# Kernel optimization log

Measured on AMD Instinct MI355X. Metric: run time of the kernel, lower is better.

Reference implementation:

```python
import jax, jax.numpy as jnp
import numpy as np

WS = 8        # window_size
SHIFT = 4     # shift_size
DS = 16       # d_state
DTR = 4       # dt_rank = ceil(hidden_dim/16)


def _win_part(x, ws):
    # (B,H,W,C) -> (B*nH*nW, ws*ws, C)
    B, H, W, C = x.shape
    x = x.reshape(B, H // ws, ws, W // ws, ws, C).transpose(0, 1, 3, 2, 4, 5)
    return x.reshape(-1, ws * ws, C)


def _win_rev(xw, ws, B, H, W):
    C = xw.shape[-1]
    x = xw.reshape(B, H // ws, W // ws, ws, ws, C).transpose(0, 1, 3, 2, 4, 5)
    return x.reshape(B, H, W, C)


def _ln(x, g, b):
    mu = x.mean(-1, keepdims=True)
    var = x.var(-1, keepdims=True)
    return (x - mu) / jnp.sqrt(var + 1e-5) * g + b


def _conv2d(v, w, b, pad):
    out = jax.lax.conv_general_dilated(v, w, (1, 1), [(pad, pad), (pad, pad)],
                                       dimension_numbers=('NCHW', 'OIHW', 'NCHW'))
    return out + b[None, :, None, None]


def setup_inputs() -> dict:
    key = jax.random.key(0)
    B, C, H, W = 2, 64, 192, 192
    di = 128  # expand * hidden_dim
    ks = jax.random.split(key, 12)

    def n(k, shape, s=0.02):
        return jax.random.normal(k, shape, jnp.float32) * s

    return {
        'x': jax.random.normal(ks[0], (B, C, H, W), jnp.float32),
        'ln1_g': jnp.ones((C,), jnp.float32), 'ln1_b': jnp.zeros((C,), jnp.float32),
        'in_w': n(ks[1], (C, 2 * di)), 'in_b': jnp.zeros((2 * di,), jnp.float32),
        'conv_w': n(ks[2], (4, di), 0.1), 'conv_b': jnp.zeros((di,), jnp.float32),
        'xproj_w': n(ks[3], (di, DTR + 2 * DS)),
        'dt_w': n(ks[4], (DTR, di), 0.1),
        'dt_b': jnp.full((di,), float(np.log(np.expm1(0.01))), jnp.float32),
        'A_log': jnp.log(jnp.tile(jnp.arange(1, DS + 1, dtype=jnp.float32), (di, 1))),
        'D': jnp.ones((di,), jnp.float32),
        'out_w': n(ks[5], (di, C)), 'out_b': jnp.zeros((C,), jnp.float32),
        'skip1': jnp.ones((C,), jnp.float32),
        'ln2_g': jnp.ones((C,), jnp.float32), 'ln2_b': jnp.zeros((C,), jnp.float32),
        'skip2': jnp.ones((C,), jnp.float32),
        'cab_w1': n(ks[6], (C // 4, C, 3, 3), 0.05), 'cab_b1': jnp.zeros((C // 4,), jnp.float32),
        'cab_w2': n(ks[7], (C, C // 4, 3, 3), 0.05), 'cab_b2': jnp.zeros((C,), jnp.float32),
        'ca_wd': n(ks[8], (C // 16, C, 1, 1), 0.05), 'ca_bd': jnp.zeros((C // 16,), jnp.float32),
        'ca_wu': n(ks[9], (C, C // 16, 1, 1), 0.05), 'ca_bu': jnp.zeros((C,), jnp.float32),
    }


def reference(x, ln1_g, ln1_b, in_w, in_b, conv_w, conv_b, xproj_w, dt_w, dt_b,
              A_log, D, out_w, out_b, skip1, ln2_g, ln2_b, skip2,
              cab_w1, cab_b1, cab_w2, cab_b2, ca_wd, ca_bd, ca_wu, ca_bu):
    B, C, H, W = x.shape
    shortcut = x.transpose(0, 2, 3, 1)  # (B,H,W,C)
    # H,W divisible by WS -> no padding, pad mask is None
    xp = jnp.roll(shortcut, (-SHIFT, -SHIFT), axis=(1, 2))
    shift_mask = jnp.zeros((B, H, W, 1), x.dtype).at[:, :H - SHIFT, :W - SHIFT, :].set(1.0)
    mask_w = _win_part(shift_mask, WS)  # (N, L, 1)

    xn = _ln(xp, ln1_g, ln1_b)
    # --- SW_HSS3D: windowed Mamba selective-scan mixer ---
    xz = xn @ in_w + in_b
    x_in, z = jnp.split(xz, 2, axis=-1)
    xw = _win_part(x_in, WS) * mask_w        # (N, L, di)
    zw = _win_part(z, WS)
    K = conv_w.shape[0]
    L = xw.shape[1]
    xpad = jnp.pad(xw, ((0, 0), (K - 1, 0), (0, 0)))  # causal depthwise conv1d
    xc = sum(xpad[:, k:k + L, :] * conv_w[k] for k in range(K)) + conv_b
    xc = jax.nn.silu(xc)
    dbc = xc @ xproj_w
    dt = jax.nn.softplus(dbc[..., :DTR] @ dt_w + dt_b)  # (N,L,di)
    Bm = dbc[..., DTR:DTR + DS]
    Cm = dbc[..., DTR + DS:]
    A = -jnp.exp(A_log)  # (di,DS)

    def step(h, t):
        dt_t, B_t, C_t, x_t = t
        h = jnp.exp(dt_t[..., None] * A) * h + (dt_t * x_t)[..., None] * B_t[:, None, :]
        y = jnp.einsum('nds,ns->nd', h, C_t)
        return h, y

    N, di = xc.shape[0], xc.shape[-1]
    h0 = jnp.zeros((N, di, DS), xc.dtype)
    xs = (dt.transpose(1, 0, 2), Bm.transpose(1, 0, 2), Cm.transpose(1, 0, 2), xc.transpose(1, 0, 2))
    _, ys = jax.lax.scan(step, h0, xs)
    y = ys.transpose(1, 0, 2) + D * xc
    y = y * jax.nn.silu(zw)
    out = y @ out_w + out_b  # (N,L,C)
    xb = _win_rev(out, WS, B, H, W)
    # NOTE: source computes roll-back but overwrites it: depad uses x_back_win directly.
    x1 = shortcut * skip1 + xb
    # --- CAB conv FFN with channel attention ---
    x2 = _ln(x1, ln2_g, ln2_b).transpose(0, 3, 1, 2)  # (B,C,H,W)
    c = _conv2d(x2, cab_w1, cab_b1, 1)
    c = jax.nn.gelu(c, approximate=False)
    c = _conv2d(c, cab_w2, cab_b2, 1)
    att = c.mean(axis=(2, 3), keepdims=True)
    att = jax.nn.relu(_conv2d(att, ca_wd, ca_bd, 0))
    att = jax.nn.sigmoid(_conv2d(att, ca_wu, ca_bu, 0))
    cab = c * att
    x_out = x1 * skip2 + cab.transpose(0, 2, 3, 1)
    return x_out.transpose(0, 3, 1, 2)
```

## Files before the change

kernel.cpp:

```cpp
#include <hip/hip_runtime.h>
#include <hip/hip_bf16.h>
#include <math.h>

#define Hh 192
#define Ww 192
#define HWp (Hh*Ww)
#define Bb 2
#define Cch 64
#define DI 128
#define NWX 24
#define WPB 576
#define NW  1152
#define DS 16
#define SHIFT 4

typedef __attribute__((ext_vector_type(8))) short short8v;
typedef __attribute__((ext_vector_type(4))) float f32x4;

__global__ __launch_bounds__(256) void k_prep(
    const float* __restrict__ in_w, const float* __restrict__ out_w,
    const float* __restrict__ w1, const float* __restrict__ w2, const float* __restrict__ xp,
    __hip_bfloat16* __restrict__ inT, __hip_bfloat16* __restrict__ outT,
    __hip_bfloat16* __restrict__ w1i, __hip_bfloat16* __restrict__ w2i,
    float* __restrict__ xpi){
  int i = blockIdx.x*256 + threadIdx.x;
  if (i < 18432) {
    int o = i/72, c = i%72;
    inT[i] = (__hip_bfloat16)((c < 64) ? in_w[c*256 + o] : 0.f);
    return;
  }
  i -= 18432;
  if (i < 8704) {
    int o = i/136, c = i%136;
    outT[i] = (__hip_bfloat16)((c < 128) ? out_w[c*64 + o] : 0.f);
    return;
  }
  i -= 8704;
  if (i < 10368) {
    int tap = i/1152, r = i%1152, co = r/72, ci = r%72;
    w1i[i] = (__hip_bfloat16)((ci < 64) ? w1[(co*64 + ci)*9 + tap] : 0.f);
    return;
  }
  i -= 10368;
  if (i < 12800) {
    int p = i/2560, r = i%2560, co = r/40, k = r%40;
    float v = 0.f;
    if (k < 32) { int tap = p*2 + (k>>4); int ci = k & 15; if (tap < 9) v = w2[co*144 + ci*9 + tap]; }
    w2i[i] = (__hip_bfloat16)v;
    return;
  }
  i -= 12800;
  if (i < 4736) {
    int c = i/37, j = i%37;
    xpi[i] = (j < 36) ? xp[c*36 + j] : 0.f;
  }
}

__global__ __launch_bounds__(256) void k_transpose(const float* __restrict__ x, float* __restrict__ xT){
  __shared__ float t[64][65];
  int b   = blockIdx.x / WPB;
  int hw0 = (blockIdx.x % WPB) * 64;
  int lane = threadIdx.x & 63, grp = threadIdx.x >> 6;
  const float* xb = x + (size_t)b * Cch * HWp;
  #pragma unroll
  for (int r = 0; r < 64; r += 4) {
    int c = r + grp;
    t[c][lane] = xb[(size_t)c * HWp + hw0 + lane];
  }
  __syncthreads();
  float* xo = xT + ((size_t)b * HWp + hw0) * 64;
  #pragma unroll
  for (int r = 0; r < 64; r += 4) {
    int hwl = r + grp;
    xo[(size_t)hwl * 64 + lane] = t[lane][hwl];
  }
}

__global__ __launch_bounds__(256) void k_stage1(
    const float* __restrict__ xT, const float* __restrict__ g1, const float* __restrict__ b1,
    const __hip_bfloat16* __restrict__ inT, const float* __restrict__ in_b,
    const float* __restrict__ conv_w, const float* __restrict__ conv_b,
    const float* __restrict__ xpi,
    __hip_bfloat16* __restrict__ xc, __hip_bfloat16* __restrict__ Zb, float* __restrict__ dbc){
  __shared__ __align__(16) __hip_bfloat16 xs[64][72];
  __shared__ __align__(16) __hip_bfloat16 wt[256][72];
  __shared__ __align__(16) float XZ[64][132];
  float* wsx = reinterpret_cast<float*>(&wt[0][0]);
  int n = blockIdx.x;
  int b = n / WPB, wi = n % WPB;
  int wy = wi / NWX, wx = wi % NWX;
  int tid = threadIdx.x;
  {
    short8v* dst = reinterpret_cast<short8v*>(&wt[0][0]);
    const short8v* src = reinterpret_cast<const short8v*>(inT);
    for (int idx = tid; idx < 2304; idx += 256) dst[idx] = src[idx];
  }
  {
    int l = tid >> 2, q = tid & 3;
    int iy = l >> 3, ix = l & 7;
    int h = wy*8 + iy, w = wx*8 + ix;
    int hs = h + SHIFT; if (hs >= Hh) hs -= Hh;
    int ws2 = w + SHIFT; if (ws2 >= Ww) ws2 -= Ww;
    const float* src = xT + ((size_t)b*HWp + (size_t)hs*Ww + ws2) * 64 + q*16;
    float v[16];
    float s1 = 0.f, s2 = 0.f;
    #pragma unroll
    for (int k = 0; k < 4; k++) {
      float4 f = *reinterpret_cast<const float4*>(src + k*4);
      v[k*4+0]=f.x; v[k*4+1]=f.y; v[k*4+2]=f.z; v[k*4+3]=f.w;
    }
    #pragma unroll
    for (int i = 0; i < 16; i++) { s1 += v[i]; s2 += v[i]*v[i]; }
    s1 += __shfl_xor(s1, 1); s2 += __shfl_xor(s2, 1);
    s1 += __shfl_xor(s1, 2); s2 += __shfl_xor(s2, 2);
    float mu = s1 * (1.f/64.f);
    float var = s2 * (1.f/64.f) - mu*mu;
    float rstd = rsqrtf(var + 1e-5f);
    __hip_bfloat16 tmp[16];
    #pragma unroll
    for (int i = 0; i < 16; i++) {
      int c = q*16 + i;
      tmp[i] = (__hip_bfloat16)((v[i]-mu)*rstd*g1[c] + b1[c]);
    }
    *reinterpret_cast<short8v*>(&xs[l][q*16])     = *reinterpret_cast<short8v*>(&tmp[0]);
    *reinterpret_cast<short8v*>(&xs[l][q*16 + 8]) = *reinterpret_cast<short8v*>(&tmp[8]);
  }
  __syncthreads();
  {
    int w = tid >> 6, lane = tid & 63;
    int col = lane & 15, g = lane >> 4;
    short8v af[4][2];
    #pragma unroll
    for (int m = 0; m < 4; m++)
      #pragma unroll
      for (int kh = 0; kh < 2; kh++)
        af[m][kh] = *reinterpret_cast<const short8v*>(&xs[m*16 + col][kh*32 + g*8]);
    f32x4 acc[4][4];
    #pragma unroll
    for (int m = 0; m < 4; m++)
      #pragma unroll
      for (int nt = 0; nt < 4; nt++)
        acc[m][nt] = (f32x4){0.f,0.f,0.f,0.f};
    #pragma unroll
    for (int nt = 0; nt < 4; nt++) {
      int o = (w*4 + nt)*16 + col;
      #pragma unroll
      for (int kh = 0; kh < 2; kh++) {
        short8v bf = *reinterpret_cast<const short8v*>(&wt[o][kh*32 + g*8]);
        #pragma unroll
        for (int m = 0; m < 4; m++)
          acc[m][nt] = __builtin_amdgcn_mfma_f32_16x16x32_bf16(af[m][kh], bf, acc[m][nt], 0, 0, 0);
      }
    }
    #pragma unroll
    for (int nt = 0; nt < 4; nt++) {
      int colg = (w*4 + nt)*16 + col;
      float bias = in_b[colg];
      #pragma unroll
      for (int m = 0; m < 4; m++) {
        #pragma unroll
        for (int j = 0; j < 4; j++) {
          int row = m*16 + g*4 + j;
          float val = acc[m][nt][j] + bias;
          if (colg < 128) XZ[row][colg] = val;
          else Zb[((size_t)n*64 + row)*128 + (colg - 128)] = (__hip_bfloat16)val;
        }
      }
    }
  }
  __syncthreads();
  {
    int d = tid & 127, half = tid >> 7;
    int t0 = half * 32;
    float cw0 = conv_w[d], cw1 = conv_w[128+d], cw2 = conv_w[256+d], cw3 = conv_w[384+d];
    float cb = conv_b[d];
    float p1 = 0.f, p2 = 0.f, p3 = 0.f;
    if (half) {
      int hh, ww2;
      hh = wy*8 + (31>>3); ww2 = wx*8 + (31&7);
      p1 = XZ[31][d] * ((hh < Hh-SHIFT && ww2 < Ww-SHIFT) ? 1.f : 0.f);
      hh = wy*8 + (30>>3); ww2 = wx*8 + (30&7);
      p2 = XZ[30][d] * ((hh < Hh-SHIFT && ww2 < Ww-SHIFT) ? 1.f : 0.f);
      hh = wy*8 + (29>>3); ww2 = wx*8 + (29&7);
      p3 = XZ[29][d] * ((hh < Hh-SHIFT && ww2 < Ww-SHIFT) ? 1.f : 0.f);
    }
    __syncthreads();
    __hip_bfloat16* Xn = xc + (size_t)n*8192;
    #pragma unroll 4
    for (int i = 0; i < 32; i++) {
      int t = t0 + i;
      int hh = wy*8 + (t>>3), ww2 = wx*8 + (t&7);
      float m = (hh < Hh-SHIFT && ww2 < Ww-SHIFT) ? 1.f : 0.f;
      float xv = XZ[t][d] * m;
      float pre = cw3*xv + cw2*p1 + cw1*p2 + cw0*p3 + cb;
      float sv = pre / (1.f + __expf(-pre));
      Xn[t*128 + d] = (__hip_bfloat16)sv;
      XZ[t][d] = sv;
      p3 = p2; p2 = p1; p1 = xv;
    }
  }
  __syncthreads();
  {
    float4* dst = reinterpret_cast<float4*>(wsx);
    const float4* src = reinterpret_cast<const float4*>(xpi);
    for (int idx = tid; idx < 1184; idx += 256) dst[idx] = src[idx];
  }
  __syncthreads();
  {
    int t = tid >> 2, jq = tid & 3;
    float acc[9];
    #pragma unroll
    for (int u = 0; u < 9; u++) acc[u] = 0.f;
    for (int c = 0; c < 128; c++) {
      float xv = XZ[t][c];
      #pragma unroll
      for (int u = 0; u < 9; u++) acc[u] += xv * wsx[c*37 + jq*9+u];
    }
    float* dst = dbc + ((size_t)n*64 + t)*36 + jq*9;
    #pragma unroll
    for (int u = 0; u < 9; u++) dst[u] = acc[u];
  }
}

__global__ __launch_bounds__(128) void k_scan3(
    __hip_bfloat16* __restrict__ xc,
    const __hip_bfloat16* __restrict__ Zb, const float* __restrict__ dbc,
    const float* __restrict__ dt_w, const float* __restrict__ dt_b,
    const float* __restrict__ A_log, const float* __restrict__ Dp){
  int n = blockIdx.x;
  int d = threadIdx.x;
  const float* Dn = dbc + (size_t)n*2304;
  float dtb  = dt_b[d];
  float dtw0 = dt_w[d], dtw1 = dt_w[128+d], dtw2 = dt_w[256+d], dtw3 = dt_w[384+d];
  float Dd = Dp[d];
  float a[16];
  bool pow_ok = true;
  #pragma unroll
  for (int s = 0; s < 16; s++) {
    a[s] = -__expf(A_log[d*16+s]);
    pow_ok = pow_ok && (__builtin_fabsf(a[s] + (float)(s+1)) < 1e-3f);
  }
  float h[16];
  #pragma unroll
  for (int s = 0; s < 16; s++) h[s] = 0.f;
  const __hip_bfloat16* Xn = xc + (size_t)n*8192;
  const __hip_bfloat16* Zn = Zb + (size_t)n*8192;
  __hip_bfloat16* Gn = xc + (size_t)n*8192;
  if (pow_ok) {
    #pragma unroll 2
    for (int i = 0; i < 64; i++) {
      const float* row = Dn + i*36;
      float4 dv = *reinterpret_cast<const float4*>(row);
      float4 B0 = *reinterpret_cast<const float4*>(row + 4);
      float4 B1 = *reinterpret_cast<const float4*>(row + 8);
      float4 B2 = *reinterpret_cast<const float4*>(row + 12);
      float4 B3 = *reinterpret_cast<const float4*>(row + 16);
      float4 C0 = *reinterpret_cast<const float4*>(row + 20);
      float4 C1 = *reinterpret_cast<const float4*>(row + 24);
      float4 C2 = *reinterpret_cast<const float4*>(row + 28);
      float4 C3 = *reinterpret_cast<const float4*>(row + 32);
      float pre = dtb + dv.x*dtw0 + dv.y*dtw1 + dv.z*dtw2 + dv.w*dtw3;
      float dtv = (pre > 15.f) ? pre : __logf(1.f + __expf(pre));
      float xcv = __bfloat162float(Xn[i*128 + d]);
      float zv  = __bfloat162float(Zn[i*128 + d]);
      float du  = dtv * xcv;
      float P[16];
      P[0] = __expf(-dtv);
      #pragma unroll
      for (int s = 1; s < 16; s++) {
        int aa = (s-1) >> 1, bb = (s-1) - aa;
        P[s] = P[aa] * P[bb];
      }
      h[0]  = P[0]*h[0]  + du*B0.x;  h[1]  = P[1]*h[1]  + du*B0.y;
      h[2]  = P[2]*h[2]  + du*B0.z;  h[3]  = P[3]*h[3]  + du*B0.w;
      h[4]  = P[4]*h[4]  + du*B1.x;  h[5]  = P[5]*h[5]  + du*B1.y;
      h[6]  = P[6]*h[6]  + du*B1.z;  h[7]  = P[7]*h[7]  + du*B1.w;
      h[8]  = P[8]*h[8]  + du*B2.x;  h[9]  = P[9]*h[9]  + du*B2.y;
      h[10] = P[10]*h[10]+ du*B2.z;  h[11] = P[11]*h[11]+ du*B2.w;
      h[12] = P[12]*h[12]+ du*B3.x;  h[13] = P[13]*h[13]+ du*B3.y;
      h[14] = P[14]*h[14]+ du*B3.z;  h[15] = P[15]*h[15]+ du*B3.w;
      float y0 = h[0]*C0.x + h[1]*C0.y;   y0 += h[2]*C0.z + h[3]*C0.w;
      float y1 = h[4]*C1.x + h[5]*C1.y;   y1 += h[6]*C1.z + h[7]*C1.w;
      float y2 = h[8]*C2.x + h[9]*C2.y;   y2 += h[10]*C2.z + h[11]*C2.w;
      float y3 = h[12]*C3.x + h[13]*C3.y; y3 += h[14]*C3.z + h[15]*C3.w;
      float y = (y0 + y1) + (y2 + y3);
      float yv = y + Dd*xcv;
      Gn[i*128 + d] = (__hip_bfloat16)(yv * (zv / (1.f + __expf(-zv))));
    }
  } else {
    #pragma unroll 2
    for (int i = 0; i < 64; i++) {
      const float* row = Dn + i*36;
      float4 dv = *reinterpret_cast<const float4*>(row);
      float pre = dtb + dv.x*dtw0 + dv.y*dtw1 + dv.z*dtw2 + dv.w*dtw3;
      float dtv = (pre > 15.f) ? pre : __logf(1.f + __expf(pre));
      float xcv = __bfloat162float(Xn[i*128 + d]);
      float zv  = __bfloat162float(Zn[i*128 + d]);
      float du  = dtv * xcv;
      float y = 0.f;
      #pragma unroll
      for (int s = 0; s < 16; s++) {
        float e = __expf(dtv * a[s]);
        h[s] = e*h[s] + du*row[4+s];
        y += h[s]*row[20+s];
      }
      float yv = y + Dd*xcv;
      Gn[i*128 + d] = (__hip_bfloat16)(yv * (zv / (1.f + __expf(-zv))));
    }
  }
}

__global__ __launch_bounds__(256) void k_out(
    const float* __restrict__ xT, const __hip_bfloat16* __restrict__ g,
    const __hip_bfloat16* __restrict__ outT, const float* __restrict__ out_b,
    const float* __restrict__ skip1, const float* __restrict__ g2, const float* __restrict__ b2,
    __hip_bfloat16* __restrict__ x1, __hip_bfloat16* __restrict__ x2){
  __shared__ __align__(16) __hip_bfloat16 gs[64][136];
  __shared__ __align__(16) __hip_bfloat16 wt[64][136];
  __shared__ float outs[64][65];
  int n = blockIdx.x;
  int b = n / WPB, wi = n % WPB;
  int wy = wi / NWX, wx = wi % NWX;
  int tid = threadIdx.x;
  {
    const short8v* src = reinterpret_cast<const short8v*>(g + (size_t)n*8192);
    for (int idx = tid; idx < 1024; idx += 256) {
      int t = idx >> 4, seg = idx & 15;
      *reinterpret_cast<short8v*>(&gs[t][seg*8]) = src[idx];
    }
  }
  {
    short8v* dst = reinterpret_cast<short8v*>(&wt[0][0]);
    const short8v* wsrc = reinterpret_cast<const short8v*>(outT);
    for (int idx = tid; idx < 1088; idx += 256) dst[idx] = wsrc[idx];
  }
  __syncthreads();
  {
    int w = tid >> 6, lane = tid & 63;
    int col = lane & 15, gq = lane >> 4;
    f32x4 acc[4] = {{0.f,0.f,0.f,0.f},{0.f,0.f,0.f,0.f},{0.f,0.f,0.f,0.f},{0.f,0.f,0.f,0.f}};
    #pragma unroll
    for (int kh = 0; kh < 4; kh++) {
      short8v af = *reinterpret_cast<const short8v*>(&gs[w*16 + col][kh*32 + gq*8]);
      #pragma unroll
      for (int nt = 0; nt < 4; nt++) {
        short8v bf = *reinterpret_cast<const short8v*>(&wt[nt*16 + col][kh*32 + gq*8]);
        acc[nt] = __builtin_amdgcn_mfma_f32_16x16x32_bf16(af, bf, acc[nt], 0, 0, 0);
      }
    }
    #pragma unroll
    for (int nt = 0; nt < 4; nt++) {
      int o = nt*16 + col;
      float bias = out_b[o];
      #pragma unroll
      for (int j = 0; j < 4; j++)
        outs[w*16 + gq*4 + j][o] = acc[nt][j] + bias;
    }
  }
  __syncthreads();
  int l = tid >> 2, q = tid & 3;
  int hh = wy*8 + (l>>3), ww2 = wx*8 + (l&7);
  size_t T = (size_t)b*HWp + (size_t)hh*Ww + ww2;
  float v[16];
  float s1 = 0.f, s2 = 0.f;
  #pragma unroll
  for (int i = 0; i < 16; i++) {
    int c = q*16 + i;
    float val = xT[T*64 + c] * skip1[c] + outs[l][c];
    v[i] = val; s1 += val; s2 += val*val;
  }
  s1 += __shfl_xor(s1, 1); s2 += __shfl_xor(s2, 1);
  s1 += __shfl_xor(s1, 2); s2 += __shfl_xor(s2, 2);
  float mu = s1*(1.f/64.f);
  float var = s2*(1.f/64.f) - mu*mu;
  float rstd = rsqrtf(var + 1e-5f);
  __hip_bfloat16 t1[16], t2[16];
  #pragma unroll
  for (int i = 0; i < 16; i++) {
    int c = q*16 + i;
    t1[i] = (__hip_bfloat16)v[i];
    t2[i] = (__hip_bfloat16)((v[i]-mu)*rstd*g2[c] + b2[c]);
  }
  *reinterpret_cast<short8v*>(&x1[T*64 + q*16])     = *reinterpret_cast<short8v*>(&t1[0]);
  *reinterpret_cast<short8v*>(&x1[T*64 + q*16 + 8]) = *reinterpret_cast<short8v*>(&t1[8]);
  *reinterpret_cast<short8v*>(&x2[T*64 + q*16])     = *reinterpret_cast<short8v*>(&t2[0]);
  *reinterpret_cast<short8v*>(&x2[T*64 + q*16 + 8]) = *reinterpret_cast<short8v*>(&t2[8]);
}

__global__ __launch_bounds__(256) void k_conv1(
    const __hip_bfloat16* __restrict__ x2, const __hip_bfloat16* __restrict__ w1i, const float* __restrict__ bc1,
    __hip_bfloat16* __restrict__ c1){
  __shared__ __align__(16) __hip_bfloat16 xt[100][72];
  __shared__ __align__(16) __hip_bfloat16 wt[9][16][72];
  int b = blockIdx.x / WPB;
  int r = blockIdx.x % WPB;
  int by = r / NWX, bx = r % NWX;
  {
    short8v* dst = reinterpret_cast<short8v*>(&wt[0][0][0]);
    const short8v* src = reinterpret_cast<const short8v*>(w1i);
    for (int idx = threadIdx.x; idx < 1296; idx += 256) dst[idx] = src[idx];
  }
  for (int idx = threadIdx.x; idx < 800; idx += 256) {
    int p = idx >> 3, seg = idx & 7;
    int gy = by*8 + p/10 - 1;
    int gx = bx*8 + p%10 - 1;
    short8v v = {0,0,0,0,0,0,0,0};
    if (gy >= 0 && gy < Hh && gx >= 0 && gx < Ww)
      v = *reinterpret_cast<const short8v*>(&x2[((size_t)b*HWp + (size_t)gy*Ww + gx)*64 + seg*8]);
    *reinterpret_cast<short8v*>(&xt[p][seg*8]) = v;
  }
  __syncthreads();
  int wv = threadIdx.x >> 6;
  int l  = threadIdx.x & 63;
  int col = l & 15, g = l >> 4;
  int apix = wv*16 + col;
  int apy = apix >> 3, apx = apix & 7;
  f32x4 acc = {0.f,0.f,0.f,0.f};
  #pragma unroll
  for (int tap = 0; tap < 9; tap++) {
    int ky = tap/3, kx = tap%3;
    const __hip_bfloat16* arow = &xt[(apy+ky)*10 + apx+kx][0];
    #pragma unroll
    for (int kh = 0; kh < 2; kh++) {
      short8v af = *reinterpret_cast<const short8v*>(&arow[kh*32 + g*8]);
      short8v bf = *reinterpret_cast<const short8v*>(&wt[tap][col][kh*32 + g*8]);
      acc = __builtin_amdgcn_mfma_f32_16x16x32_bf16(af, bf, acc, 0, 0, 0);
    }
  }
  float bias = bc1[col];
  #pragma unroll
  for (int j = 0; j < 4; j++) {
    int opix = wv*16 + g*4 + j;
    int oy = by*8 + (opix>>3), ox = bx*8 + (opix&7);
    float v = acc[j] + bias;
    float gv = 0.5f * v * (1.f + erff(v * 0.70710678118f));
    c1[((size_t)b*HWp + (size_t)oy*Ww + ox)*16 + col] = (__hip_bfloat16)gv;
  }
}

__global__ __launch_bounds__(256) void k_conv2(
    const __hip_bfloat16* __restrict__ c1, const __hip_bfloat16* __restrict__ w2i, const float* __restrict__ bc2,
    __hip_bfloat16* __restrict__ c2, float* __restrict__ sums){
  __shared__ __align__(16) __hip_bfloat16 xt[100][16];
  __shared__ __align__(16) __hip_bfloat16 wt[5][64][40];
  __shared__ float red[4][64];
  int b = blockIdx.x / WPB;
  int r = blockIdx.x % WPB;
  int by = r / NWX, bx = r % NWX;
  {
    short8v* dst = reinterpret_cast<short8v*>(&wt[0][0][0]);
    const short8v* src = reinterpret_cast<const short8v*>(w2i);
    for (int idx = threadIdx.x; idx < 1600; idx += 256) dst[idx] = src[idx];
  }
  for (int idx = threadIdx.x; idx < 400; idx += 256) {
    int p = idx >> 2, c4 = idx & 3;
    int gy = by*8 + p/10 - 1;
    int gx = bx*8 + p%10 - 1;
    ushort4 v = {0,0,0,0};
    if (gy >= 0 && gy < Hh && gx >= 0 && gx < Ww)
      v = *reinterpret_cast<const ushort4*>(&c1[((size_t)b*HWp + (size_t)gy*Ww + gx)*16 + c4*4]);
    *reinterpret_cast<ushort4*>(&xt[p][c4*4]) = v;
  }
  __syncthreads();
  int wv4 = threadIdx.x >> 6;
  int l   = threadIdx.x & 63;
  int col = l & 15, g = l >> 4;
  int apix = wv4*16 + col;
  int apy = apix >> 3, apx = apix & 7;
  f32x4 acc[4] = {{0.f,0.f,0.f,0.f},{0.f,0.f,0.f,0.f},{0.f,0.f,0.f,0.f},{0.f,0.f,0.f,0.f}};
  #pragma unroll
  for (int p = 0; p < 5; p++) {
    int tap = p*2 + (g >> 1); if (tap > 8) tap = 8;
    int ky = tap/3, kx = tap%3;
    short8v af = *reinterpret_cast<const short8v*>(&xt[(apy+ky)*10 + apx+kx][(g&1)*8]);
    #pragma unroll
    for (int ct = 0; ct < 4; ct++) {
      short8v bf = *reinterpret_cast<const short8v*>(&wt[p][ct*16 + col][g*8]);
      acc[ct] = __builtin_amdgcn_mfma_f32_16x16x32_bf16(af, bf, acc[ct], 0, 0, 0);
    }
  }
  #pragma unroll
  for (int ct = 0; ct < 4; ct++) {
    int co = ct*16 + col;
    float bias = bc2[co];
    float part = 0.f;
    #pragma unroll
    for (int j = 0; j < 4; j++) {
      int opix = wv4*16 + g*4 + j;
      int oy = by*8 + (opix>>3), ox = bx*8 + (opix&7);
      float v = acc[ct][j] + bias;
      c2[((size_t)b*HWp + (size_t)oy*Ww + ox)*64 + co] = (__hip_bfloat16)v;
      part += v;
    }
    part += __shfl_xor(part, 16);
    part += __shfl_xor(part, 32);
    if (g == 0) red[wv4][co] = part;
  }
  __syncthreads();
  if (threadIdx.x < 64) {
    float s = red[0][threadIdx.x] + red[1][threadIdx.x] + red[2][threadIdx.x] + red[3][threadIdx.x];
    atomicAdd(&sums[b*64 + threadIdx.x], s);
  }
}

__global__ void k_att(const float* __restrict__ sums,
                      const float* __restrict__ wd, const float* __restrict__ bd,
                      const float* __restrict__ wu, const float* __restrict__ bu,
                      float* __restrict__ att){
  int tid = threadIdx.x;
  int b = tid >> 6, co = tid & 63;
  float inv = 1.f / (float)HWp;
  float hid[4];
  #pragma unroll
  for (int j = 0; j < 4; j++) {
    float acc = bd[j];
    for (int c = 0; c < 64; c++) acc += wd[j*64+c] * (sums[b*64+c] * inv);
    hid[j] = fmaxf(acc, 0.f);
  }
  float acc = bu[co];
  #pragma unroll
  for (int j = 0; j < 4; j++) acc += wu[co*4+j] * hid[j];
  att[tid] = 1.f / (1.f + __expf(-acc));
}

__global__ __launch_bounds__(256) void k_final(
    const __hip_bfloat16* __restrict__ x1, const __hip_bfloat16* __restrict__ c2,
    const float* __restrict__ skip2, const float* __restrict__ att,
    float* __restrict__ out){
  __shared__ float t[64][65];
  int b = blockIdx.x / WPB;
  int hw0 = (blockIdx.x % WPB) * 64;
  int lane = threadIdx.x & 63, grp = threadIdx.x >> 6;
  float sk = skip2[lane], at = att[b*64 + lane];
  #pragma unroll
  for (int r = 0; r < 64; r += 4) {
    int hwl = r + grp;
    size_t T = (size_t)b*HWp + hw0 + hwl;
    float xv = __bfloat162float(x1[T*64+lane]);
    float cv = __bfloat162float(c2[T*64+lane]);
    t[hwl][lane] = xv*sk + cv*at;
  }
  __syncthreads();
  float* ob = out + (size_t)b * Cch * HWp;
  #pragma unroll
  for (int r = 0; r < 64; r += 4) {
    int c = r + grp;
    ob[(size_t)c*HWp + hw0 + lane] = t[lane][c];
  }
}

extern "C" void kernel_launch(void* const* d_in, const int* in_sizes, int n_in,
                              void* d_out, int out_size, void* d_ws, size_t ws_size,
                              hipStream_t stream) {
  (void)in_sizes; (void)n_in; (void)out_size; (void)ws_size;
  const float* x      = (const float*)d_in[0];
  const float* ln1_g  = (const float*)d_in[1];
  const float* ln1_b  = (const float*)d_in[2];
  const float* in_w   = (const float*)d_in[3];
  const float* in_b   = (const float*)d_in[4];
  const float* conv_w = (const float*)d_in[5];
  const float* conv_b = (const float*)d_in[6];
  const float* xproj_w= (const float*)d_in[7];
  const float* dt_w   = (const float*)d_in[8];
  const float* dt_b   = (const float*)d_in[9];
  const float* A_log  = (const float*)d_in[10];
  const float* Dp     = (const float*)d_in[11];
  const float* out_w  = (const float*)d_in[12];
  const float* out_b  = (const float*)d_in[13];
  const float* skip1  = (const float*)d_in[14];
  const float* ln2_g  = (const float*)d_in[15];
  const float* ln2_b  = (const float*)d_in[16];
  const float* skip2  = (const float*)d_in[17];
  const float* cab_w1 = (const float*)d_in[18];
  const float* cab_b1 = (const float*)d_in[19];
  const float* cab_w2 = (const float*)d_in[20];
  const float* cab_b2 = (const float*)d_in[21];
  const float* ca_wd  = (const float*)d_in[22];
  const float* ca_bd  = (const float*)d_in[23];
  const float* ca_wu  = (const float*)d_in[24];
  const float* ca_bu  = (const float*)d_in[25];

  float* ws   = (float*)d_ws;
  float* xT   = ws;
  __hip_bfloat16* xc = (__hip_bfloat16*)(ws + 4718592);
  __hip_bfloat16* z  = (__hip_bfloat16*)(ws + 14155776);
  float* dbc  = ws + 23592960;
  float* sums = ws + 26247168;
  float* att  = ws + 26247296;
  __hip_bfloat16* x1 = (__hip_bfloat16*)(ws + 14155776);
  __hip_bfloat16* x2 = (__hip_bfloat16*)(ws + 18874368);
  __hip_bfloat16* c1 = (__hip_bfloat16*)(ws + 23592960);
  __hip_bfloat16* c2 = (__hip_bfloat16*)(ws + 4718592);
  __hip_bfloat16* inT  = (__hip_bfloat16*)(ws + 26247424);
  __hip_bfloat16* outT = (__hip_bfloat16*)(ws + 26256640);
  __hip_bfloat16* w1i  = (__hip_bfloat16*)(ws + 26260992);
  __hip_bfloat16* w2i  = (__hip_bfloat16*)(ws + 26266176);
  float*          xpi  = ws + 26272576;

  hipMemsetAsync(sums, 0, 128*sizeof(float), stream);
  k_prep<<<215, 256, 0, stream>>>(in_w, out_w, cab_w1, cab_w2, xproj_w,
                                  inT, outT, w1i, w2i, xpi);
  k_transpose<<<NW, 256, 0, stream>>>(x, xT);
  k_stage1<<<NW, 256, 0, stream>>>(xT, ln1_g, ln1_b, inT, in_b, conv_w, conv_b, xpi,
                                   xc, z, dbc);
  k_scan3<<<NW, 128, 0, stream>>>(xc, z, dbc, dt_w, dt_b, A_log, Dp);
  k_out<<<NW, 256, 0, stream>>>(xT, xc, outT, out_b, skip1, ln2_g, ln2_b, x1, x2);
  k_conv1<<<NW, 256, 0, stream>>>(x2, w1i, cab_b1, c1);
  k_conv2<<<NW, 256, 0, stream>>>(c1, w2i, cab_b2, c2, sums);
  k_att<<<1, 128, 0, stream>>>(sums, ca_wd, ca_bd, ca_wu, ca_bu, att);
  k_final<<<NW, 256, 0, stream>>>(x1, c2, skip2, att, (float*)d_out);
}
```

Before: 184.8 us.

## Store transposed input as bf16, fold attention into final kernel, drop memset

The transposed NHWC copy of x is now written in bf16 rather than fp32, halving its write in k_transpose and its reads in k_stage1 and k_out. The tiny channel-attention kernel is removed and each k_final block recomputes the attention vector for its batch in shared memory. The memset of the sums buffer is folded into k_prep. Together these cut two launches and some memory traffic, at the cost of bf16 rounding on the residual shortcut and redundant attention math in every block.

```diff
diff --git a/kernel.cpp b/kernel.cpp
--- a/kernel.cpp
+++ b/kernel.cpp
@@ -22,7 +22,7 @@
     const float* __restrict__ w1, const float* __restrict__ w2, const float* __restrict__ xp,
     __hip_bfloat16* __restrict__ inT, __hip_bfloat16* __restrict__ outT,
     __hip_bfloat16* __restrict__ w1i, __hip_bfloat16* __restrict__ w2i,
-    float* __restrict__ xpi){
+    float* __restrict__ xpi, float* __restrict__ sums){
   int i = blockIdx.x*256 + threadIdx.x;
   if (i < 18432) {
     int o = i/72, c = i%72;
@@ -53,10 +53,13 @@
   if (i < 4736) {
     int c = i/37, j = i%37;
     xpi[i] = (j < 36) ? xp[c*36 + j] : 0.f;
-  }
-}
-
-__global__ __launch_bounds__(256) void k_transpose(const float* __restrict__ x, float* __restrict__ xT){
+    return;
+  }
+  i -= 4736;
+  if (i < 128) sums[i] = 0.f;
+}
+
+__global__ __launch_bounds__(256) void k_transpose(const float* __restrict__ x, __hip_bfloat16* __restrict__ xT){
   __shared__ float t[64][65];
   int b   = blockIdx.x / WPB;
   int hw0 = (blockIdx.x % WPB) * 64;
@@ -68,16 +71,16 @@
     t[c][lane] = xb[(size_t)c * HWp + hw0 + lane];
   }
   __syncthreads();
-  float* xo = xT + ((size_t)b * HWp + hw0) * 64;
+  __hip_bfloat16* xo = xT + ((size_t)b * HWp + hw0) * 64;
   #pragma unroll
   for (int r = 0; r < 64; r += 4) {
     int hwl = r + grp;
-    xo[(size_t)hwl * 64 + lane] = t[lane][hwl];
+    xo[(size_t)hwl * 64 + lane] = (__hip_bfloat16)t[lane][hwl];
   }
 }
 
 __global__ __launch_bounds__(256) void k_stage1(
-    const float* __restrict__ xT, const float* __restrict__ g1, const float* __restrict__ b1,
+    const __hip_bfloat16* __restrict__ xT, const float* __restrict__ g1, const float* __restrict__ b1,
     const __hip_bfloat16* __restrict__ inT, const float* __restrict__ in_b,
     const float* __restrict__ conv_w, const float* __restrict__ conv_b,
     const float* __restrict__ xpi,
@@ -101,16 +104,14 @@
     int h = wy*8 + iy, w = wx*8 + ix;
     int hs = h + SHIFT; if (hs >= Hh) hs -= Hh;
     int ws2 = w + SHIFT; if (ws2 >= Ww) ws2 -= Ww;
-    const float* src = xT + ((size_t)b*HWp + (size_t)hs*Ww + ws2) * 64 + q*16;
+    const __hip_bfloat16* src = xT + ((size_t)b*HWp + (size_t)hs*Ww + ws2) * 64 + q*16;
+    __hip_bfloat16 tv[16];
+    *reinterpret_cast<short8v*>(&tv[0]) = *reinterpret_cast<const short8v*>(src);
+    *reinterpret_cast<short8v*>(&tv[8]) = *reinterpret_cast<const short8v*>(src + 8);
     float v[16];
     float s1 = 0.f, s2 = 0.f;
     #pragma unroll
-    for (int k = 0; k < 4; k++) {
-      float4 f = *reinterpret_cast<const float4*>(src + k*4);
-      v[k*4+0]=f.x; v[k*4+1]=f.y; v[k*4+2]=f.z; v[k*4+3]=f.w;
-    }
-    #pragma unroll
-    for (int i = 0; i < 16; i++) { s1 += v[i]; s2 += v[i]*v[i]; }
+    for (int i = 0; i < 16; i++) { v[i] = __bfloat162float(tv[i]); s1 += v[i]; s2 += v[i]*v[i]; }
     s1 += __shfl_xor(s1, 1); s2 += __shfl_xor(s2, 1);
     s1 += __shfl_xor(s1, 2); s2 += __shfl_xor(s2, 2);
     float mu = s1 * (1.f/64.f);
@@ -311,7 +312,7 @@
 }
 
 __global__ __launch_bounds__(256) void k_out(
-    const float* __restrict__ xT, const __hip_bfloat16* __restrict__ g,
+    const __hip_bfloat16* __restrict__ xT, const __hip_bfloat16* __restrict__ g,
     const __hip_bfloat16* __restrict__ outT, const float* __restrict__ out_b,
     const float* __restrict__ skip1, const float* __restrict__ g2, const float* __restrict__ b2,
     __hip_bfloat16* __restrict__ x1, __hip_bfloat16* __restrict__ x2){
@@ -361,12 +362,15 @@
   int l = tid >> 2, q = tid & 3;
   int hh = wy*8 + (l>>3), ww2 = wx*8 + (l&7);
   size_t T = (size_t)b*HWp + (size_t)hh*Ww + ww2;
+  __hip_bfloat16 sc[16];
+  *reinterpret_cast<short8v*>(&sc[0]) = *reinterpret_cast<const short8v*>(&xT[T*64 + q*16]);
+  *reinterpret_cast<short8v*>(&sc[8]) = *reinterpret_cast<const short8v*>(&xT[T*64 + q*16 + 8]);
   float v[16];
   float s1 = 0.f, s2 = 0.f;
   #pragma unroll
   for (int i = 0; i < 16; i++) {
     int c = q*16 + i;
-    float val = xT[T*64 + c] * skip1[c] + outs[l][c];
+    float val = __bfloat162float(sc[i]) * skip1[c] + outs[l][c];
     v[i] = val; s1 += val; s2 += val*val;
   }
   s1 += __shfl_xor(s1, 1); s2 += __shfl_xor(s2, 1);
@@ -503,35 +507,35 @@
   }
 }
 
-__global__ void k_att(const float* __restrict__ sums,
-                      const float* __restrict__ wd, const float* __restrict__ bd,
-                      const float* __restrict__ wu, const float* __restrict__ bu,
-                      float* __restrict__ att){
-  int tid = threadIdx.x;
-  int b = tid >> 6, co = tid & 63;
-  float inv = 1.f / (float)HWp;
-  float hid[4];
-  #pragma unroll
-  for (int j = 0; j < 4; j++) {
-    float acc = bd[j];
-    for (int c = 0; c < 64; c++) acc += wd[j*64+c] * (sums[b*64+c] * inv);
-    hid[j] = fmaxf(acc, 0.f);
-  }
-  float acc = bu[co];
-  #pragma unroll
-  for (int j = 0; j < 4; j++) acc += wu[co*4+j] * hid[j];
-  att[tid] = 1.f / (1.f + __expf(-acc));
-}
-
 __global__ __launch_bounds__(256) void k_final(
     const __hip_bfloat16* __restrict__ x1, const __hip_bfloat16* __restrict__ c2,
-    const float* __restrict__ skip2, const float* __restrict__ att,
+    const float* __restrict__ skip2, const float* __restrict__ sums,
+    const float* __restrict__ wd, const float* __restrict__ bd,
+    const float* __restrict__ wu, const float* __restrict__ bu,
     float* __restrict__ out){
   __shared__ float t[64][65];
+  __shared__ float hid_s[4];
+  __shared__ float att_s[64];
   int b = blockIdx.x / WPB;
   int hw0 = (blockIdx.x % WPB) * 64;
   int lane = threadIdx.x & 63, grp = threadIdx.x >> 6;
-  float sk = skip2[lane], at = att[b*64 + lane];
+  if (threadIdx.x < 4) {
+    int j = threadIdx.x;
+    float inv = 1.f / (float)HWp;
+    float acc = bd[j];
+    for (int c = 0; c < 64; c++) acc += wd[j*64+c] * (sums[b*64+c] * inv);
+    hid_s[j] = fmaxf(acc, 0.f);
+  }
+  __syncthreads();
+  if (threadIdx.x < 64) {
+    int co = threadIdx.x;
+    float acc = bu[co];
+    #pragma unroll
+    for (int j = 0; j < 4; j++) acc += wu[co*4+j] * hid_s[j];
+    att_s[co] = 1.f / (1.f + __expf(-acc));
+  }
+  __syncthreads();
+  float sk = skip2[lane], at = att_s[lane];
   #pragma unroll
   for (int r = 0; r < 64; r += 4) {
     int hwl = r + grp;
@@ -581,12 +585,11 @@
   const float* ca_bu  = (const float*)d_in[25];
 
   float* ws   = (float*)d_ws;
-  float* xT   = ws;
+  __hip_bfloat16* xT = (__hip_bfloat16*)ws;
   __hip_bfloat16* xc = (__hip_bfloat16*)(ws + 4718592);
   __hip_bfloat16* z  = (__hip_bfloat16*)(ws + 14155776);
   float* dbc  = ws + 23592960;
   float* sums = ws + 26247168;
-  float* att  = ws + 26247296;
   __hip_bfloat16* x1 = (__hip_bfloat16*)(ws + 14155776);
   __hip_bfloat16* x2 = (__hip_bfloat16*)(ws + 18874368);
   __hip_bfloat16* c1 = (__hip_bfloat16*)(ws + 23592960);
@@ -597,9 +600,8 @@
   __hip_bfloat16* w2i  = (__hip_bfloat16*)(ws + 26266176);
   float*          xpi  = ws + 26272576;
 
-  hipMemsetAsync(sums, 0, 128*sizeof(float), stream);
-  k_prep<<<215, 256, 0, stream>>>(in_w, out_w, cab_w1, cab_w2, xproj_w,
-                                  inT, outT, w1i, w2i, xpi);
+  k_prep<<<216, 256, 0, stream>>>(in_w, out_w, cab_w1, cab_w2, xproj_w,
+                                  inT, outT, w1i, w2i, xpi, sums);
   k_transpose<<<NW, 256, 0, stream>>>(x, xT);
   k_stage1<<<NW, 256, 0, stream>>>(xT, ln1_g, ln1_b, inT, in_b, conv_w, conv_b, xpi,
                                    xc, z, dbc);
@@ -607,6 +609,6 @@
   k_out<<<NW, 256, 0, stream>>>(xT, xc, outT, out_b, skip1, ln2_g, ln2_b, x1, x2);
   k_conv1<<<NW, 256, 0, stream>>>(x2, w1i, cab_b1, c1);
   k_conv2<<<NW, 256, 0, stream>>>(c1, w2i, cab_b2, c2, sums);
-  k_att<<<1, 128, 0, stream>>>(sums, ca_wd, ca_bd, ca_wu, ca_bu, att);
-  k_final<<<NW, 256, 0, stream>>>(x1, c2, skip2, att, (float*)d_out);
-}
+  k_final<<<NW, 256, 0, stream>>>(x1, c2, skip2, sums, ca_wd, ca_bd, ca_wu, ca_bu,
+                                  (float*)d_out);
+}
```

New measurement: 175.7 us (median of 2 runs). 1.05x faster.
